# Optimization experiments

Measured on AMD Instinct MI355X. Metric: run time of the kernel, lower is better.

## Reference

```python
import jax, jax.numpy as jnp
import numpy as np

N, E = 8192, 16384
IN_C, HID = 64, 64
ALPHA, BETA = -1.5, -0.5
DENSITY = 0.004


def setup_inputs() -> dict:
    key = jax.random.key(0)
    k_x, k_b, k_w0, k_w1 = jax.random.split(key, 4)
    x_0 = jax.random.normal(k_x, (N, IN_C), dtype=jnp.float32)
    # sparse binary incidence matrix (stored dense, as in the original module)
    B1 = (jax.random.uniform(k_b, (N, E)) < DENSITY).astype(jnp.float32)
    # guarantee every node and every hyperedge has at least one incidence
    B1 = B1.at[jnp.arange(N), jnp.arange(N) % E].set(1.0)
    B1 = B1.at[jnp.arange(E) % N, jnp.arange(E)].set(1.0)
    W0 = jax.random.normal(k_w0, (IN_C, HID), dtype=jnp.float32) * (1.0 / np.sqrt(IN_C))
    W1 = jax.random.normal(k_w1, (HID, HID), dtype=jnp.float32) * (1.0 / np.sqrt(HID))
    bias_0_to_1 = jnp.zeros((1, HID), dtype=jnp.float32)
    bias_1_to_0 = jnp.zeros((1, HID), dtype=jnp.float32)
    return {"x_0": x_0, "incidence_1": B1, "W0": W0, "W1": W1,
            "bias_0_to_1": bias_0_to_1, "bias_1_to_0": bias_1_to_0}


def _normalize_incidence(B1):
    # vectorized equivalent of the O(N*E) python double loop
    mask = (B1 != 0).astype(B1.dtype)                  # [N,E]
    edge_sum = B1.sum(axis=0)                          # [E] hyperedge sizes
    node_sum = B1.sum(axis=1)                          # [N] node degrees
    edge_norm = edge_sum ** ALPHA                      # [E]
    node_norm = node_sum ** BETA                       # [N]
    # edge_factor[i] = 1 / sum_j mask[i,j]*edge_norm[j]  (row mat-vec)
    row_fac = 1.0 / (mask @ edge_norm)                 # [N]
    # node_factor[j] = 1 / sum_i mask[i,j]*node_norm[i]  (col mat-vec)
    col_fac = 1.0 / (mask.T @ node_norm)               # [E]
    return B1 * (row_fac * node_norm)[:, None] * (edge_norm * col_fac)[None, :]


def reference(x_0, incidence_1, W0, W1, bias_0_to_1, bias_1_to_0):
    B = _normalize_incidence(incidence_1)              # [N,E]
    # conv 0 -> 1: x_1 = B^T @ (x_0 @ W0) + b
    x_1 = B.T @ (x_0 @ W0) + bias_0_to_1               # [E,HID]
    # conv 1 -> 0: x_0' = B @ (x_1 @ W1) + b
    x_0_out = B @ (x_1 @ W1) + bias_1_to_0             # [N,HID]
    return jax.nn.relu(x_0_out), jax.nn.relu(x_1)
```

## Files before the change

### kernel.cpp

```cpp
#include <hip/hip_runtime.h>
#include <hip/hip_bf16.h>
#include <stdint.h>

#define NN 8192
#define NE 16384
#define RCAP 128
#define CCAP 96

#define OFF_COLCNT   0u
#define MEMSET_BYTES (NE*4u)
#define OFF_ROWCNT   MEMSET_BYTES
#define OFF_RSCALE   (OFF_ROWCNT + NN*4u)
#define OFF_CSCALE   (OFF_RSCALE + NN*4u)
#define OFF_CSR      (OFF_CSCALE + NE*4u)
#define OFF_CSC      (OFF_CSR + NN*RCAP*4u)
#define OFF_Y0       (OFF_CSC + NE*CCAP*4u)
#define OFF_X1PRE    (OFF_Y0 + NN*64*4u)
#define OFF_Z1       (OFF_X1PRE + NE*64*4u)

__global__ __launch_bounds__(256) void k_scan(const float* __restrict__ B1,
        uint32_t* __restrict__ row_cnt, uint32_t* __restrict__ col_cnt,
        uint32_t* __restrict__ csr_col, uint32_t* __restrict__ csc_row) {
    __shared__ uint32_t rcur;
    const int tid = threadIdx.x;
    const int i = blockIdx.x;
    if (tid == 0) rcur = 0;
    __syncthreads();
    const long long base = (long long)i * NE;
    for (int it = 0; it < 16; ++it) {
        int local = it * 1024 + tid * 4;
        float4 v = *reinterpret_cast<const float4*>(B1 + base + local);
        float vs[4] = {v.x, v.y, v.z, v.w};
        #pragma unroll
        for (int q = 0; q < 4; ++q) {
            if (vs[q] != 0.0f) {
                uint32_t j = (uint32_t)(local + q);
                uint32_t p = atomicAdd(&rcur, 1u);
                if (p < RCAP) csr_col[(uint32_t)i * RCAP + p] = j;
                uint32_t qq = atomicAdd(&col_cnt[j], 1u);
                if (qq < CCAP) csc_row[j * CCAP + qq] = (uint32_t)i;
            }
        }
    }
    __syncthreads();
    if (tid == 0) row_cnt[i] = (rcur < RCAP) ? rcur : RCAP;
}

__global__ __launch_bounds__(256) void k_scales(
        const uint32_t* __restrict__ row_cnt, const uint32_t* __restrict__ col_cnt,
        const uint32_t* __restrict__ csr_col, const uint32_t* __restrict__ csc_row,
        float* __restrict__ rowscale, float* __restrict__ colscale) {
    int w = blockIdx.x * 4 + (threadIdx.x >> 6);
    int lane = threadIdx.x & 63;
    float s = 0.f;
    if (w < NN) {
        uint32_t c = row_cnt[w];
        const uint32_t* p = csr_col + (uint32_t)w * RCAP;
        for (uint32_t t = lane; t < c; t += 64) {
            float cj = (float)col_cnt[p[t]];
            s += 1.0f / (cj * sqrtf(cj));
        }
        #pragma unroll
        for (int off = 32; off >= 1; off >>= 1) s += __shfl_xor(s, off);
        if (lane == 0) rowscale[w] = 1.0f / (sqrtf((float)c) * s);
    } else {
        int j = w - NN;
        uint32_t c = col_cnt[j];
        uint32_t cl = c > CCAP ? CCAP : c;
        const uint32_t* p = csc_row + (uint32_t)j * CCAP;
        for (uint32_t t = lane; t < cl; t += 64) {
            float ri = (float)row_cnt[p[t]];
            s += 1.0f / sqrtf(ri);
        }
        #pragma unroll
        for (int off = 32; off >= 1; off >>= 1) s += __shfl_xor(s, off);
        float cf = (float)c;
        if (lane == 0) colscale[j] = 1.0f / (cf * sqrtf(cf) * s);
    }
}

__global__ __launch_bounds__(256) void k_gemm64(const float* __restrict__ X,
        const float* __restrict__ W, const float* __restrict__ scale,
        float* __restrict__ Y) {
    __shared__ float ws[64 * 64];
    __shared__ float xs[4][64];
    int tid = threadIdx.x;
    int c = tid & 63, rr = tid >> 6;
    for (int k = tid; k < 4096; k += 256) ws[k] = W[k];
    int row0 = blockIdx.x * 4;
    xs[rr][c] = X[(row0 + rr) * 64 + c];
    __syncthreads();
    float acc = 0.f;
    #pragma unroll
    for (int k = 0; k < 64; ++k) acc = fmaf(xs[rr][k], ws[k * 64 + c], acc);
    Y[(row0 + rr) * 64 + c] = scale[row0 + rr] * acc;
}

__global__ __launch_bounds__(256) void k_edge_gather(
        const uint32_t* __restrict__ col_cnt, const uint32_t* __restrict__ csc_row,
        const float* __restrict__ colscale, const float* __restrict__ y0s,
        const float* __restrict__ bias01, float* __restrict__ x1pre,
        float* __restrict__ out1) {
    int w = threadIdx.x >> 6, lane = threadIdx.x & 63;
    int j = blockIdx.x * 4 + w;
    uint32_t e = col_cnt[j]; if (e > CCAP) e = CCAP;
    const uint32_t* p = csc_row + (uint32_t)j * CCAP;
    int g = lane >> 4, fl = lane & 15;
    float4 acc = make_float4(0.f, 0.f, 0.f, 0.f);
    for (uint32_t t = g; t < e; t += 4) {
        uint32_t i = p[t];
        const float4 v = *reinterpret_cast<const float4*>(y0s + i * 64u + fl * 4);
        acc.x += v.x; acc.y += v.y; acc.z += v.z; acc.w += v.w;
    }
    acc.x += __shfl_xor(acc.x, 16); acc.y += __shfl_xor(acc.y, 16);
    acc.z += __shfl_xor(acc.z, 16); acc.w += __shfl_xor(acc.w, 16);
    acc.x += __shfl_xor(acc.x, 32); acc.y += __shfl_xor(acc.y, 32);
    acc.z += __shfl_xor(acc.z, 32); acc.w += __shfl_xor(acc.w, 32);
    if (g == 0) {
        float cs = colscale[j];
        const float4 bb = *reinterpret_cast<const float4*>(bias01 + fl * 4);
        float4 val = make_float4(fmaf(cs, acc.x, bb.x), fmaf(cs, acc.y, bb.y),
                                 fmaf(cs, acc.z, bb.z), fmaf(cs, acc.w, bb.w));
        *reinterpret_cast<float4*>(x1pre + j * 64u + fl * 4) = val;
        float4 r = make_float4(fmaxf(val.x, 0.f), fmaxf(val.y, 0.f),
                               fmaxf(val.z, 0.f), fmaxf(val.w, 0.f));
        *reinterpret_cast<float4*>(out1 + j * 64u + fl * 4) = r;
    }
}

__global__ __launch_bounds__(256) void k_node_gather(
        const uint32_t* __restrict__ row_cnt, const uint32_t* __restrict__ csr_col,
        const float* __restrict__ rowscale, const float* __restrict__ z1s,
        const float* __restrict__ bias10, float* __restrict__ out0) {
    int w = threadIdx.x >> 6, lane = threadIdx.x & 63;
    int i = blockIdx.x * 4 + w;
    uint32_t e = row_cnt[i];
    const uint32_t* p = csr_col + (uint32_t)i * RCAP;
    int g = lane >> 4, fl = lane & 15;
    float4 acc = make_float4(0.f, 0.f, 0.f, 0.f);
    for (uint32_t t = g; t < e; t += 4) {
        uint32_t jj = p[t];
        const float4 v = *reinterpret_cast<const float4*>(z1s + jj * 64u + fl * 4);
        acc.x += v.x; acc.y += v.y; acc.z += v.z; acc.w += v.w;
    }
    acc.x += __shfl_xor(acc.x, 16); acc.y += __shfl_xor(acc.y, 16);
    acc.z += __shfl_xor(acc.z, 16); acc.w += __shfl_xor(acc.w, 16);
    acc.x += __shfl_xor(acc.x, 32); acc.y += __shfl_xor(acc.y, 32);
    acc.z += __shfl_xor(acc.z, 32); acc.w += __shfl_xor(acc.w, 32);
    if (g == 0) {
        float rs = rowscale[i];
        const float4 bb = *reinterpret_cast<const float4*>(bias10 + fl * 4);
        float4 val = make_float4(fmaf(rs, acc.x, bb.x), fmaf(rs, acc.y, bb.y),
                                 fmaf(rs, acc.z, bb.z), fmaf(rs, acc.w, bb.w));
        float4 r = make_float4(fmaxf(val.x, 0.f), fmaxf(val.y, 0.f),
                               fmaxf(val.z, 0.f), fmaxf(val.w, 0.f));
        *reinterpret_cast<float4*>(out0 + i * 64u + fl * 4) = r;
    }
}

extern "C" void kernel_launch(void* const* d_in, const int* in_sizes, int n_in,
                              void* d_out, int out_size, void* d_ws, size_t ws_size,
                              hipStream_t stream) {
    const float* x0  = (const float*)d_in[0];
    const float* B1  = (const float*)d_in[1];
    const float* W0  = (const float*)d_in[2];
    const float* W1  = (const float*)d_in[3];
    const float* b01 = (const float*)d_in[4];
    const float* b10 = (const float*)d_in[5];
    float* out = (float*)d_out;
    char* ws = (char*)d_ws;

    uint32_t* col_cnt = (uint32_t*)(ws + OFF_COLCNT);
    uint32_t* row_cnt = (uint32_t*)(ws + OFF_ROWCNT);
    float*    rscale  = (float*)(ws + OFF_RSCALE);
    float*    cscale  = (float*)(ws + OFF_CSCALE);
    uint32_t* csr_col = (uint32_t*)(ws + OFF_CSR);
    uint32_t* csc_row = (uint32_t*)(ws + OFF_CSC);
    float*    y0      = (float*)(ws + OFF_Y0);
    float*    x1pre   = (float*)(ws + OFF_X1PRE);
    float*    z1      = (float*)(ws + OFF_Z1);

    hipMemsetAsync(col_cnt, 0, MEMSET_BYTES, stream);

    k_scan<<<NN, 256, 0, stream>>>(B1, row_cnt, col_cnt, csr_col, csc_row);
    k_scales<<<(NN + NE) / 4, 256, 0, stream>>>(row_cnt, col_cnt, csr_col, csc_row,
            rscale, cscale);
    k_gemm64<<<NN / 4, 256, 0, stream>>>(x0, W0, rscale, y0);
    k_edge_gather<<<NE / 4, 256, 0, stream>>>(col_cnt, csc_row, cscale, y0,
            b01, x1pre, out + NN * 64);
    k_gemm64<<<NE / 4, 256, 0, stream>>>(x1pre, W1, cscale, z1);
    k_node_gather<<<NN / 4, 256, 0, stream>>>(row_cnt, csr_col, rscale, z1, b10, out);
}
```

Baseline: 766.9 us.

## Fuse x0·W0 into scan kernel and W1 GEMM into edge gather

The first dense GEMM now runs as extra blocks of the incidence-scan kernel, and the row scaling is applied in the scales kernel. The second GEMM is fused into the edge-gather kernel through a shared-memory tile, which removes the x1pre intermediate and two launches. B1 is read with nontemporal loads to avoid polluting the cache. The cost is that every edge block reloads W1 into shared memory and adds a block-wide barrier.

```diff
diff --git a/kernel.cpp b/kernel.cpp
--- a/kernel.cpp
+++ b/kernel.cpp
@@ -6,6 +6,8 @@
 #define NE 16384
 #define RCAP 128
 #define CCAP 96
+
+typedef float f32x4 __attribute__((ext_vector_type(4)));
 
 #define OFF_COLCNT   0u
 #define MEMSET_BYTES (NE*4u)
@@ -15,41 +17,59 @@
 #define OFF_CSR      (OFF_CSCALE + NE*4u)
 #define OFF_CSC      (OFF_CSR + NN*RCAP*4u)
 #define OFF_Y0       (OFF_CSC + NE*CCAP*4u)
-#define OFF_X1PRE    (OFF_Y0 + NN*64*4u)
-#define OFF_Z1       (OFF_X1PRE + NE*64*4u)
-
-__global__ __launch_bounds__(256) void k_scan(const float* __restrict__ B1,
+#define OFF_Z1       (OFF_Y0 + NN*64*4u)
+
+__global__ __launch_bounds__(256) void k_scan_gemm(const float* __restrict__ B1,
+        const float* __restrict__ x0, const float* __restrict__ W0,
         uint32_t* __restrict__ row_cnt, uint32_t* __restrict__ col_cnt,
-        uint32_t* __restrict__ csr_col, uint32_t* __restrict__ csc_row) {
+        uint32_t* __restrict__ csr_col, uint32_t* __restrict__ csc_row,
+        float* __restrict__ y0) {
+    __shared__ float wsm[64 * 64];
+    __shared__ float xs[4][64];
     __shared__ uint32_t rcur;
     const int tid = threadIdx.x;
-    const int i = blockIdx.x;
-    if (tid == 0) rcur = 0;
-    __syncthreads();
-    const long long base = (long long)i * NE;
-    for (int it = 0; it < 16; ++it) {
-        int local = it * 1024 + tid * 4;
-        float4 v = *reinterpret_cast<const float4*>(B1 + base + local);
-        float vs[4] = {v.x, v.y, v.z, v.w};
-        #pragma unroll
-        for (int q = 0; q < 4; ++q) {
-            if (vs[q] != 0.0f) {
-                uint32_t j = (uint32_t)(local + q);
-                uint32_t p = atomicAdd(&rcur, 1u);
-                if (p < RCAP) csr_col[(uint32_t)i * RCAP + p] = j;
-                uint32_t qq = atomicAdd(&col_cnt[j], 1u);
-                if (qq < CCAP) csc_row[j * CCAP + qq] = (uint32_t)i;
+    if (blockIdx.x < NN) {
+        const int i = blockIdx.x;
+        if (tid == 0) rcur = 0;
+        __syncthreads();
+        const long long base = (long long)i * NE;
+        for (int it = 0; it < 16; ++it) {
+            int local = it * 1024 + tid * 4;
+            f32x4 v = __builtin_nontemporal_load(
+                    reinterpret_cast<const f32x4*>(B1 + base + local));
+            #pragma unroll
+            for (int q = 0; q < 4; ++q) {
+                if (v[q] != 0.0f) {
+                    uint32_t j = (uint32_t)(local + q);
+                    uint32_t p = atomicAdd(&rcur, 1u);
+                    if (p < RCAP) csr_col[(uint32_t)i * RCAP + p] = j;
+                    uint32_t qq = atomicAdd(&col_cnt[j], 1u);
+                    if (qq < CCAP) csc_row[j * CCAP + qq] = (uint32_t)i;
+                }
             }
         }
-    }
-    __syncthreads();
-    if (tid == 0) row_cnt[i] = (rcur < RCAP) ? rcur : RCAP;
+        __syncthreads();
+        if (tid == 0) row_cnt[i] = (rcur < RCAP) ? rcur : RCAP;
+    } else {
+        int c = tid & 63, rr = tid >> 6;
+        for (int k = tid * 4; k < 4096; k += 1024)
+            *reinterpret_cast<f32x4*>(wsm + k) =
+                *reinterpret_cast<const f32x4*>(W0 + k);
+        int row0 = (blockIdx.x - NN) * 4;
+        xs[rr][c] = x0[(row0 + rr) * 64 + c];
+        __syncthreads();
+        float acc = 0.f;
+        #pragma unroll
+        for (int k = 0; k < 64; ++k) acc = fmaf(xs[rr][k], wsm[k * 64 + c], acc);
+        y0[(row0 + rr) * 64 + c] = acc;
+    }
 }
 
 __global__ __launch_bounds__(256) void k_scales(
         const uint32_t* __restrict__ row_cnt, const uint32_t* __restrict__ col_cnt,
         const uint32_t* __restrict__ csr_col, const uint32_t* __restrict__ csc_row,
-        float* __restrict__ rowscale, float* __restrict__ colscale) {
+        float* __restrict__ rowscale, float* __restrict__ colscale,
+        float* __restrict__ y0) {
     int w = blockIdx.x * 4 + (threadIdx.x >> 6);
     int lane = threadIdx.x & 63;
     float s = 0.f;
@@ -62,7 +82,9 @@
         }
         #pragma unroll
         for (int off = 32; off >= 1; off >>= 1) s += __shfl_xor(s, off);
-        if (lane == 0) rowscale[w] = 1.0f / (sqrtf((float)c) * s);
+        float rs = 1.0f / (sqrtf((float)c) * s);
+        y0[w * 64 + lane] *= rs;
+        if (lane == 0) rowscale[w] = rs;
     } else {
         int j = w - NN;
         uint32_t c = col_cnt[j];
@@ -79,29 +101,18 @@
     }
 }
 
-__global__ __launch_bounds__(256) void k_gemm64(const float* __restrict__ X,
-        const float* __restrict__ W, const float* __restrict__ scale,
-        float* __restrict__ Y) {
-    __shared__ float ws[64 * 64];
-    __shared__ float xs[4][64];
-    int tid = threadIdx.x;
-    int c = tid & 63, rr = tid >> 6;
-    for (int k = tid; k < 4096; k += 256) ws[k] = W[k];
-    int row0 = blockIdx.x * 4;
-    xs[rr][c] = X[(row0 + rr) * 64 + c];
-    __syncthreads();
-    float acc = 0.f;
-    #pragma unroll
-    for (int k = 0; k < 64; ++k) acc = fmaf(xs[rr][k], ws[k * 64 + c], acc);
-    Y[(row0 + rr) * 64 + c] = scale[row0 + rr] * acc;
-}
-
-__global__ __launch_bounds__(256) void k_edge_gather(
+__global__ __launch_bounds__(256) void k_edge_fused(
         const uint32_t* __restrict__ col_cnt, const uint32_t* __restrict__ csc_row,
         const float* __restrict__ colscale, const float* __restrict__ y0s,
-        const float* __restrict__ bias01, float* __restrict__ x1pre,
-        float* __restrict__ out1) {
-    int w = threadIdx.x >> 6, lane = threadIdx.x & 63;
+        const float* __restrict__ bias01, const float* __restrict__ W1,
+        float* __restrict__ z1s, float* __restrict__ out1) {
+    __shared__ float w1s[64 * 64];
+    __shared__ float xrow[4][64];
+    int tid = threadIdx.x;
+    for (int k = tid * 4; k < 4096; k += 1024)
+        *reinterpret_cast<f32x4*>(w1s + k) =
+            *reinterpret_cast<const f32x4*>(W1 + k);
+    int w = tid >> 6, lane = tid & 63;
     int j = blockIdx.x * 4 + w;
     uint32_t e = col_cnt[j]; if (e > CCAP) e = CCAP;
     const uint32_t* p = csc_row + (uint32_t)j * CCAP;
@@ -121,11 +132,16 @@
         const float4 bb = *reinterpret_cast<const float4*>(bias01 + fl * 4);
         float4 val = make_float4(fmaf(cs, acc.x, bb.x), fmaf(cs, acc.y, bb.y),
                                  fmaf(cs, acc.z, bb.z), fmaf(cs, acc.w, bb.w));
-        *reinterpret_cast<float4*>(x1pre + j * 64u + fl * 4) = val;
+        *reinterpret_cast<float4*>(&xrow[w][fl * 4]) = val;
         float4 r = make_float4(fmaxf(val.x, 0.f), fmaxf(val.y, 0.f),
                                fmaxf(val.z, 0.f), fmaxf(val.w, 0.f));
         *reinterpret_cast<float4*>(out1 + j * 64u + fl * 4) = r;
     }
+    __syncthreads();
+    float z = 0.f;
+    #pragma unroll
+    for (int k = 0; k < 64; ++k) z = fmaf(xrow[w][k], w1s[k * 64 + lane], z);
+    z1s[j * 64 + lane] = colscale[j] * z;
 }
 
 __global__ __launch_bounds__(256) void k_node_gather(
@@ -150,10 +166,10 @@
     if (g == 0) {
         float rs = rowscale[i];
         const float4 bb = *reinterpret_cast<const float4*>(bias10 + fl * 4);
-        float4 val = make_float4(fmaf(rs, acc.x, bb.x), fmaf(rs, acc.y, bb.y),
-                                 fmaf(rs, acc.z, bb.z), fmaf(rs, acc.w, bb.w));
-        float4 r = make_float4(fmaxf(val.x, 0.f), fmaxf(val.y, 0.f),
-                               fmaxf(val.z, 0.f), fmaxf(val.w, 0.f));
+        float4 r = make_float4(fmaxf(fmaf(rs, acc.x, bb.x), 0.f),
+                               fmaxf(fmaf(rs, acc.y, bb.y), 0.f),
+                               fmaxf(fmaf(rs, acc.z, bb.z), 0.f),
+                               fmaxf(fmaf(rs, acc.w, bb.w), 0.f));
         *reinterpret_cast<float4*>(out0 + i * 64u + fl * 4) = r;
     }
 }
@@ -177,17 +193,15 @@
     uint32_t* csr_col = (uint32_t*)(ws + OFF_CSR);
     uint32_t* csc_row = (uint32_t*)(ws + OFF_CSC);
     float*    y0      = (float*)(ws + OFF_Y0);
-    float*    x1pre   = (float*)(ws + OFF_X1PRE);
     float*    z1      = (float*)(ws + OFF_Z1);
 
     hipMemsetAsync(col_cnt, 0, MEMSET_BYTES, stream);
 
-    k_scan<<<NN, 256, 0, stream>>>(B1, row_cnt, col_cnt, csr_col, csc_row);
+    k_scan_gemm<<<NN + NN / 4, 256, 0, stream>>>(B1, x0, W0, row_cnt, col_cnt,
+            csr_col, csc_row, y0);
     k_scales<<<(NN + NE) / 4, 256, 0, stream>>>(row_cnt, col_cnt, csr_col, csc_row,
-            rscale, cscale);
-    k_gemm64<<<NN / 4, 256, 0, stream>>>(x0, W0, rscale, y0);
-    k_edge_gather<<<NE / 4, 256, 0, stream>>>(col_cnt, csc_row, cscale, y0,
-            b01, x1pre, out + NN * 64);
-    k_gemm64<<<NE / 4, 256, 0, stream>>>(x1pre, W1, cscale, z1);
+            rscale, cscale, y0);
+    k_edge_fused<<<NE / 4, 256, 0, stream>>>(col_cnt, csc_row, cscale, y0,
+            b01, W1, z1, out + NN * 64);
     k_node_gather<<<NN / 4, 256, 0, stream>>>(row_cnt, csr_col, rscale, z1, b10, out);
 }
```

Result: no change. 757.8 us (-1.2%).
